# Performance work log

Hardware: AMD Instinct MI355X
Metric: run time of the kernel (lower is better)

The kernel has to match this reference:

```python
import jax, jax.numpy as jnp
import numpy as np

B, S, F_IN, E, H, NIT = 256, 196, 384, 384, 8, 10
FH = E                      # hidden_features defaults to embed_dim
EH = E // H                 # embed dim per head = 48
FHH = FH // H               # hidden features per head = 48
OSEQ = S                    # hidden_seq_len defaults to seq_len
MIN_POS = 1e-6
W_THRESH = 1e-5


def _l1(x, axis=-1, eps=1e-12):
    # F.normalize(p=1): x / max(sum|x|, eps)
    return x / jnp.clip(jnp.sum(jnp.abs(x), axis=axis, keepdims=True), eps, None)


def _norm_weight(w):
    # normalize_weights(): L1-normalize, clamp at threshold, L1-normalize again
    w = _l1(w, axis=-1)
    w = jnp.clip(w, W_THRESH, None)
    return _l1(w, axis=-1)


def setup_inputs() -> dict:
    key = jax.random.key(0)
    ks = jax.random.split(key, 7)
    x = jax.random.normal(ks[0], (B, S, F_IN), dtype=jnp.float32)
    # h init: torch.rand in _reset_h (uniform positive)
    h0 = jax.random.uniform(ks[1], (B, OSEQ, H, FHH), dtype=jnp.float32)
    embed_w = jax.random.normal(ks[2], (E, F_IN), dtype=jnp.float32) * 0.05
    embed_b = jnp.zeros((E,), dtype=jnp.float32)
    local_weight = _norm_weight(jax.random.uniform(ks[3], (FHH, EH), dtype=jnp.float32))
    global_weight = _norm_weight(jax.random.uniform(ks[4], (H, OSEQ, S), dtype=jnp.float32))
    out_w = jax.random.normal(ks[5], (F_IN, E), dtype=jnp.float32) * 0.05
    out_b = jnp.zeros((F_IN,), dtype=jnp.float32)
    return {"x": x, "h0": h0, "embed_w": embed_w, "embed_b": embed_b,
            "local_weight": local_weight, "global_weight": global_weight,
            "out_w": out_w, "out_b": out_b}


def reference(x, h0, embed_w, embed_b, local_weight, global_weight, out_w, out_b):
    # embed + clamp + split heads: [B,S,H,EH]
    xe = jnp.clip(x @ embed_w.T + embed_b, MIN_POS, None)
    xe = xe.reshape(B, S, H, EH)
    # _prepare_input: L1 normalize over last dim (eps=1e-20); nonneg so |x|=x
    inp = xe / jnp.clip(jnp.sum(xe, axis=-1, keepdims=True), 1e-20, None)
    # h init, L1-normalized
    h = _l1(h0, axis=-1)

    def nnmf_forward(t):  # t: [B,S(=i),H,EH]
        t = jnp.einsum('bihe,fe->bihf', t, local_weight)          # F.linear(x, local_weight)
        return jnp.einsum('bihf,hoi->bohf', t, global_weight)     # [B,O,H,FHH]

    def nnmf_reconstruct(hh):  # hh: [B,O,H,FHH]
        t = jnp.einsum('bohf,hoi->bihf', hh, global_weight)
        return jnp.einsum('bihf,fe->bihe', t, local_weight)       # F.linear(., local_weight.t())

    # fixed-point NNMF iterations (h_update_rate=1)
    for _ in range(NIT):
        rec = jnp.clip(nnmf_reconstruct(h), MIN_POS, None)   # secure tensor
        rec = _l1(rec, axis=-1)                              # normalize_reconstruction
        h = h * nnmf_forward(inp / rec)                      # multiplicative update
        h = jnp.clip(h, MIN_POS, None)                       # _secure_tensor
        h = h / jnp.sum(h, axis=-1, keepdims=True)           # PowerSoftmax(power=1)

    # output = 'hidden': flatten heads, project back to features
    out = h.reshape(B, OSEQ, FH)
    return out @ out_w.T + out_b
```

## Files before the change

kernel.cpp:

```cpp
#include <hip/hip_runtime.h>
#include <stdint.h>

#define NB   256
#define NS   196
#define NF   384
#define NH   8
#define NEH  48
#define NIT  10
#define SP   224
#define EP   64
#define NBH  2048
#define NBS  50176
#define NT   13

using f32x4  = __attribute__((ext_vector_type(4))) float;
using u16x8  = __attribute__((ext_vector_type(8))) uint16_t;
using u16x4  = __attribute__((ext_vector_type(4))) uint16_t;
using bf16x8 = __attribute__((ext_vector_type(8))) __bf16;

static __device__ __forceinline__ float bf2f(uint16_t u){
  union { uint32_t u32; float f; } c; c.u32 = (uint32_t)u << 16; return c.f;
}
static __device__ __forceinline__ uint16_t f2bf(float f){
  __bf16 h = (__bf16)f;
  return __builtin_bit_cast(uint16_t, h);
}
static __device__ __forceinline__ float frcp(float f){
  return __builtin_amdgcn_rcpf(f);
}
static __device__ __forceinline__ bf16x8 ld8(const uint16_t* p){
  return __builtin_bit_cast(bf16x8, *(const u16x8*)p);
}
static __device__ __forceinline__ void lds_fence(){
  asm volatile("s_waitcnt lgkmcnt(0)" ::: "memory");
}
static __device__ __forceinline__ float dpp_add16(float x){
  int v = __builtin_bit_cast(int, x);
  x += __builtin_bit_cast(float, __builtin_amdgcn_update_dpp(0, v, 0xB1, 0xF, 0xF, false));
  v = __builtin_bit_cast(int, x);
  x += __builtin_bit_cast(float, __builtin_amdgcn_update_dpp(0, v, 0x4E, 0xF, 0xF, false));
  v = __builtin_bit_cast(int, x);
  x += __builtin_bit_cast(float, __builtin_amdgcn_update_dpp(0, v, 0x141, 0xF, 0xF, false));
  v = __builtin_bit_cast(int, x);
  x += __builtin_bit_cast(float, __builtin_amdgcn_update_dpp(0, v, 0x140, 0xF, 0xF, false));
  return x;
}
#define MFMA16(a,b,c) __builtin_amdgcn_mfma_f32_16x16x32_bf16((a),(b),(c),0,0,0)


__global__ void k_prep_gw(const float* __restrict__ gw, uint16_t* __restrict__ gw_b,
                          uint16_t* __restrict__ gwt_b){
  int idx = blockIdx.x * 256 + threadIdx.x;
  if (idx >= NH*SP*SP) return;
  int h = idx / (SP*SP);
  int r = (idx / SP) % SP;
  int c = idx % SP;
  float v = (r < NS && c < NS) ? gw[((size_t)h*NS + r)*NS + c] : 0.f;
  uint16_t bv = f2bf(v);
  gw_b[idx] = bv;
  gwt_b[((size_t)h*SP + c)*SP + r] = bv;
}

__global__ void k_prep_small(const float* __restrict__ lw, const float* __restrict__ ew,
                             const float* __restrict__ ow,
                             uint16_t* __restrict__ lw_b, uint16_t* __restrict__ lwt_b,
                             uint16_t* __restrict__ ew_b, uint16_t* __restrict__ ow_b){
  int idx = blockIdx.x * 256 + threadIdx.x;
  if (idx < EP*EP){
    int f = idx >> 6, e = idx & 63;
    float v = (f < NEH && e < NEH) ? lw[f*NEH + e] : 0.f;
    uint16_t bv = f2bf(v);
    lw_b[f*EP + e] = bv;
    lwt_b[e*EP + f] = bv;
  }
  if (idx < NF*NF){
    ew_b[idx] = f2bf(ew[idx]);
    ow_b[idx] = f2bf(ow[idx]);
  }
}

__global__ __launch_bounds__(512) void k_embed(const float* __restrict__ x,
    const uint16_t* __restrict__ ew_b, const float* __restrict__ eb,
    uint16_t* __restrict__ inp_fm){
  const int wave = threadIdx.x >> 6, lane = threadIdx.x & 63;
  const int lg = lane >> 4, li = lane & 15;
  const int mt = wave >> 1, nh = wave & 1;
  const int m0 = blockIdx.x * 64 + mt * 16;
  f32x4 acc[12];
  #pragma unroll
  for (int i = 0; i < 12; ++i) acc[i] = (f32x4)0.0f;
  const float* ap = x + (size_t)(m0 + li) * NF + 8*lg;
  for (int kt = 0; kt < 12; ++kt){
    f32x4 a0 = *(const f32x4*)(ap + kt*32);
    f32x4 a1 = *(const f32x4*)(ap + kt*32 + 4);
    u16x8 au;
    #pragma unroll
    for (int j = 0; j < 4; ++j){ au[j] = f2bf(a0[j]); au[j+4] = f2bf(a1[j]); }
    bf16x8 a = __builtin_bit_cast(bf16x8, au);
    #pragma unroll
    for (int nt = 0; nt < 12; ++nt){
      bf16x8 b = ld8(ew_b + (size_t)((nh*12 + nt)*16 + li)*NF + kt*32 + 8*lg);
      acc[nt] = MFMA16(a, b, acc[nt]);
    }
  }
  const int mbase = m0 + 4*lg;
  const int b  = mbase / NS;
  const int si = mbase - b*NS;
  const int t  = si >> 4, wi = si & 15;
  const int lanep = (wi >> 2)*16 + li;
  #pragma unroll
  for (int hl = 0; hl < 4; ++hl){
    int hh = nh*4 + hl;
    float xec[3][4];
    float s[4] = {0.f, 0.f, 0.f, 0.f};
    #pragma unroll
    for (int j = 0; j < 3; ++j){
      int nt = hl*3 + j;
      float bias = eb[(nh*12 + nt)*16 + li];
      #pragma unroll
      for (int r = 0; r < 4; ++r){
        float v = fmaxf(acc[nt][r] + bias, 1e-6f);
        xec[j][r] = v; s[r] += v;
      }
    }
    #pragma unroll
    for (int r = 0; r < 4; ++r) s[r] = frcp(dpp_add16(s[r]));
    uint16_t* dst = inp_fm + ((size_t)((b*NH + hh)*NT + t)*64 + lanep)*12;
    #pragma unroll
    for (int j = 0; j < 3; ++j){
      u16x4 w;
      #pragma unroll
      for (int r = 0; r < 4; ++r) w[r] = f2bf(xec[j][r] * s[r]);
      *(u16x4*)(dst + j*4) = w;
    }
  }
}

__global__ __launch_bounds__(448) void k_main(
    const float*    __restrict__ h0,
    const uint16_t* __restrict__ gw_b,
    const uint16_t* __restrict__ gwt_b,
    const uint16_t* __restrict__ lw_b,
    const uint16_t* __restrict__ lwt_b,
    const uint16_t* __restrict__ inp_fm,
    uint16_t* __restrict__ h_b)
{
  __shared__ __align__(16) uint16_t hlT[48][232];
  __shared__ __align__(16) uint16_t t2T[48][232];
  __shared__ __align__(16) uint16_t Sg[7][2][16][72];

  const int bh = blockIdx.x;
  const int b  = bh >> 3;
  const int hh = bh & 7;
  const int tid = threadIdx.x;
  const int wave = tid >> 6;
  const int lane = tid & 63;
  const int lg = lane >> 4;
  const int li = lane & 15;
  const int tt[2] = {wave, wave + 7};

  {
    u16x4 z = {0,0,0,0};
    *(u16x4*)&Sg[wave][0][li][48 + 4*lg] = z;
    *(u16x4*)&Sg[wave][1][li][48 + 4*lg] = z;
  }

  bf16x8 lwtF[3][2], lwF[3][2];
  #pragma unroll
  for (int nt = 0; nt < 3; ++nt)
    #pragma unroll
    for (int kt = 0; kt < 2; ++kt){
      lwtF[nt][kt] = ld8(lwt_b + (size_t)(nt*16 + li)*EP + kt*32 + 8*lg);
      lwF [nt][kt] = ld8(lw_b  + (size_t)(nt*16 + li)*EP + kt*32 + 8*lg);
    }

  u16x4 ip[2][3];
  #pragma unroll
  for (int tp = 0; tp < 2; ++tp){
    const int t = tt[tp];
    if (t < NT){
      const uint16_t* ipp = inp_fm + ((size_t)(bh*NT + t)*64 + lg*16 + li)*12;
      ip[tp][0] = *(const u16x4*)(ipp);
      ip[tp][1] = *(const u16x4*)(ipp + 4);
      ip[tp][2] = *(const u16x4*)(ipp + 8);
    } else {
      u16x4 z = {0,0,0,0};
      ip[tp][0] = z; ip[tp][1] = z; ip[tp][2] = z;
    }
  }

  float hr[2][3][4];
  #pragma unroll
  for (int tp = 0; tp < 2; ++tp){
    const int t = tt[tp];
    float s[4] = {0.f,0.f,0.f,0.f};
    #pragma unroll
    for (int nt = 0; nt < 3; ++nt)
      #pragma unroll
      for (int r = 0; r < 4; ++r){
        int row = t*16 + 4*lg + r;
        float v = 0.f;
        if (row < NS)
          v = h0[(((size_t)(b*NS + row))*NH + hh)*NEH + nt*16 + li];
        hr[tp][nt][r] = v;
        s[r] += fabsf(v);
      }
    #pragma unroll
    for (int r = 0; r < 4; ++r) s[r] = frcp(fmaxf(dpp_add16(s[r]), 1e-12f));
    #pragma unroll
    for (int nt = 0; nt < 3; ++nt)
      #pragma unroll
      for (int r = 0; r < 4; ++r){
        hr[tp][nt][r] *= s[r];
        Sg[wave][tp][4*lg + r][nt*16 + li] = f2bf(hr[tp][nt][r]);
      }
  }
  lds_fence();
  #pragma unroll
  for (int tp = 0; tp < 2; ++tp){
    const int t = tt[tp];
    f32x4 hl[3];
    #pragma unroll
    for (int i = 0; i < 3; ++i) hl[i] = (f32x4)0.0f;
    #pragma unroll
    for (int kt = 0; kt < 2; ++kt){
      bf16x8 a = ld8(&Sg[wave][tp][li][kt*32 + 8*lg]);
      #pragma unroll
      for (int nt = 0; nt < 3; ++nt) hl[nt] = MFMA16(a, lwtF[nt][kt], hl[nt]);
    }
    #pragma unroll
    for (int nt = 0; nt < 3; ++nt){
      u16x4 w;
      #pragma unroll
      for (int r = 0; r < 4; ++r) w[r] = f2bf(hl[nt][r]);
      *(u16x4*)&hlT[nt*16 + li][t*16 + 4*lg] = w;
    }
  }

  const uint16_t* __restrict__ gwh  = gw_b  + (size_t)hh * SP * SP;
  const uint16_t* __restrict__ gwth = gwt_b + (size_t)hh * SP * SP;
  const uint16_t* gA0t = gwth + (size_t)(tt[0]*16 + li)*SP + 8*lg;
  const uint16_t* gA1t = gwth + (size_t)(tt[1]*16 + li)*SP + 8*lg;
  const uint16_t* gA0  = gwh  + (size_t)(tt[0]*16 + li)*SP + 8*lg;
  const uint16_t* gA1  = gwh  + (size_t)(tt[1]*16 + li)*SP + 8*lg;
  __syncthreads();

  for (int it = 0; it < NIT; ++it){
    f32x4 rec[2][3];
    #pragma unroll
    for (int tp = 0; tp < 2; ++tp)
      #pragma unroll
      for (int i = 0; i < 3; ++i) rec[tp][i] = (f32x4)0.0f;
    #pragma unroll
    for (int kt = 0; kt < 7; ++kt){
      bf16x8 b0 = ld8(&hlT[ 0 + li][kt*32 + 8*lg]);
      bf16x8 b1 = ld8(&hlT[16 + li][kt*32 + 8*lg]);
      bf16x8 b2 = ld8(&hlT[32 + li][kt*32 + 8*lg]);
      bf16x8 a0 = ld8(gA0t + kt*32);
      bf16x8 a1 = ld8(gA1t + kt*32);
      rec[0][0] = MFMA16(a0, b0, rec[0][0]);
      rec[0][1] = MFMA16(a0, b1, rec[0][1]);
      rec[0][2] = MFMA16(a0, b2, rec[0][2]);
      rec[1][0] = MFMA16(a1, b0, rec[1][0]);
      rec[1][1] = MFMA16(a1, b1, rec[1][1]);
      rec[1][2] = MFMA16(a1, b2, rec[1][2]);
    }
    #pragma unroll
    for (int tp = 0; tp < 2; ++tp){
      float s[4] = {0.f,0.f,0.f,0.f};
      float rv[3][4];
      #pragma unroll
      for (int nt = 0; nt < 3; ++nt)
        #pragma unroll
        for (int r = 0; r < 4; ++r){
          float v = fmaxf(rec[tp][nt][r], 1e-6f);
          rv[nt][r] = v; s[r] += v;
        }
      #pragma unroll
      for (int r = 0; r < 4; ++r) s[r] = dpp_add16(s[r]);
      #pragma unroll
      for (int r = 0; r < 4; ++r){
        Sg[wave][tp][4*lg + r][ 0 + li] = f2bf(bf2f(ip[tp][0][r]) * s[r] * frcp(rv[0][r]));
        Sg[wave][tp][4*lg + r][16 + li] = f2bf(bf2f(ip[tp][1][r]) * s[r] * frcp(rv[1][r]));
        Sg[wave][tp][4*lg + r][32 + li] = f2bf(bf2f(ip[tp][2][r]) * s[r] * frcp(rv[2][r]));
      }
    }
    lds_fence();
    #pragma unroll
    for (int tp = 0; tp < 2; ++tp){
      const int t = tt[tp];
      f32x4 t2[3];
      #pragma unroll
      for (int i = 0; i < 3; ++i) t2[i] = (f32x4)0.0f;
      #pragma unroll
      for (int kt = 0; kt < 2; ++kt){
        bf16x8 a = ld8(&Sg[wave][tp][li][kt*32 + 8*lg]);
        #pragma unroll
        for (int nt = 0; nt < 3; ++nt) t2[nt] = MFMA16(a, lwF[nt][kt], t2[nt]);
      }
      #pragma unroll
      for (int nt = 0; nt < 3; ++nt){
        u16x4 w;
        #pragma unroll
        for (int r = 0; r < 4; ++r) w[r] = f2bf(t2[nt][r]);
        *(u16x4*)&t2T[nt*16 + li][t*16 + 4*lg] = w;
      }
    }
    __syncthreads();

    f32x4 hu[2][3];
    #pragma unroll
    for (int tp = 0; tp < 2; ++tp)
      #pragma unroll
      for (int i = 0; i < 3; ++i) hu[tp][i] = (f32x4)0.0f;
    #pragma unroll
    for (int kt = 0; kt < 7; ++kt){
      bf16x8 b0 = ld8(&t2T[ 0 + li][kt*32 + 8*lg]);
      bf16x8 b1 = ld8(&t2T[16 + li][kt*32 + 8*lg]);
      bf16x8 b2 = ld8(&t2T[32 + li][kt*32 + 8*lg]);
      bf16x8 a0 = ld8(gA0 + kt*32);
      bf16x8 a1 = ld8(gA1 + kt*32);
      hu[0][0] = MFMA16(a0, b0, hu[0][0]);
      hu[0][1] = MFMA16(a0, b1, hu[0][1]);
      hu[0][2] = MFMA16(a0, b2, hu[0][2]);
      hu[1][0] = MFMA16(a1, b0, hu[1][0]);
      hu[1][1] = MFMA16(a1, b1, hu[1][1]);
      hu[1][2] = MFMA16(a1, b2, hu[1][2]);
    }
    #pragma unroll
    for (int tp = 0; tp < 2; ++tp){
      float s[4] = {0.f,0.f,0.f,0.f};
      #pragma unroll
      for (int nt = 0; nt < 3; ++nt)
        #pragma unroll
        for (int r = 0; r < 4; ++r){
          float v = fmaxf(hr[tp][nt][r] * hu[tp][nt][r], 1e-6f);
          hr[tp][nt][r] = v; s[r] += v;
        }
      #pragma unroll
      for (int r = 0; r < 4; ++r) s[r] = frcp(dpp_add16(s[r]));
      #pragma unroll
      for (int nt = 0; nt < 3; ++nt)
        #pragma unroll
        for (int r = 0; r < 4; ++r){
          hr[tp][nt][r] *= s[r];
          Sg[wave][tp][4*lg + r][nt*16 + li] = f2bf(hr[tp][nt][r]);
        }
    }
    lds_fence();
    #pragma unroll
    for (int tp = 0; tp < 2; ++tp){
      const int t = tt[tp];
      f32x4 hl[3];
      #pragma unroll
      for (int i = 0; i < 3; ++i) hl[i] = (f32x4)0.0f;
      #pragma unroll
      for (int kt = 0; kt < 2; ++kt){
        bf16x8 a = ld8(&Sg[wave][tp][li][kt*32 + 8*lg]);
        #pragma unroll
        for (int nt = 0; nt < 3; ++nt) hl[nt] = MFMA16(a, lwtF[nt][kt], hl[nt]);
      }
      #pragma unroll
      for (int nt = 0; nt < 3; ++nt){
        u16x4 w;
        #pragma unroll
        for (int r = 0; r < 4; ++r) w[r] = f2bf(hl[nt][r]);
        *(u16x4*)&hlT[nt*16 + li][t*16 + 4*lg] = w;
      }
    }
    __syncthreads();
  }

  uint16_t* __restrict__ hrow = h_b + (size_t)bh * SP * EP;
  #pragma unroll
  for (int tp = 0; tp < 2; ++tp){
    const int t = tt[tp];
    #pragma unroll
    for (int nt = 0; nt < 3; ++nt)
      #pragma unroll
      for (int r = 0; r < 4; ++r){
        int row = t*16 + 4*lg + r;
        if (row < NS)
          hrow[(size_t)row*EP + nt*16 + li] = f2bf(hr[tp][nt][r]);
      }
  }
}

__global__ __launch_bounds__(512) void k_out(const uint16_t* __restrict__ h_b,
    const uint16_t* __restrict__ ow_b, const float* __restrict__ obv,
    float* __restrict__ out){
  const int wave = threadIdx.x >> 6, lane = threadIdx.x & 63;
  const int lg = lane >> 4, li = lane & 15;
  const int p = wave >> 2, q = wave & 3;
  const int m0 = blockIdx.x * 64;
  f32x4 acc[2][6];
  #pragma unroll
  for (int mtl = 0; mtl < 2; ++mtl)
    #pragma unroll
    for (int i = 0; i < 6; ++i) acc[mtl][i] = (f32x4)0.0f;
  size_t rowbase[2];
  #pragma unroll
  for (int mtl = 0; mtl < 2; ++mtl){
    int m = m0 + (2*p + mtl)*16 + li;
    int b = m / NS, si = m - b*NS;
    rowbase[mtl] = ((size_t)b*NH*SP + si)*EP;
  }
  for (int kt = 0; kt < 12; ++kt){
    int ks = kt*32 + 8*lg;
    int hh = ks / NEH, f = ks - hh*NEH;
    size_t koff = (size_t)hh*SP*EP + f;
    bf16x8 a0 = ld8(h_b + rowbase[0] + koff);
    bf16x8 a1 = ld8(h_b + rowbase[1] + koff);
    #pragma unroll
    for (int n = 0; n < 6; ++n){
      bf16x8 bb = ld8(ow_b + (size_t)((6*q + n)*16 + li)*NF + kt*32 + 8*lg);
      acc[0][n] = MFMA16(a0, bb, acc[0][n]);
      acc[1][n] = MFMA16(a1, bb, acc[1][n]);
    }
  }
  #pragma unroll
  for (int mtl = 0; mtl < 2; ++mtl){
    #pragma unroll
    for (int n = 0; n < 6; ++n){
      int col = (6*q + n)*16 + li;
      float bias = obv[col];
      #pragma unroll
      for (int r = 0; r < 4; ++r)
        out[(size_t)(m0 + (2*p + mtl)*16 + 4*lg + r)*NF + col] = acc[mtl][n][r] + bias;
    }
  }
}

extern "C" void kernel_launch(void* const* d_in, const int* in_sizes, int n_in,
                              void* d_out, int out_size, void* d_ws, size_t ws_size,
                              hipStream_t stream){
  const float* x   = (const float*)d_in[0];
  const float* h0  = (const float*)d_in[1];
  const float* ew  = (const float*)d_in[2];
  const float* eb  = (const float*)d_in[3];
  const float* lw  = (const float*)d_in[4];
  const float* gw  = (const float*)d_in[5];
  const float* ow  = (const float*)d_in[6];
  const float* obv = (const float*)d_in[7];
  float* out = (float*)d_out;

  char* w = (char*)d_ws;
  size_t o_inp = 0;
  size_t o_hb  = o_inp + (size_t)NBH*NT*64*12*2;
  size_t o_gw  = o_hb  + (size_t)NBH*SP*EP*2;
  size_t o_gwt = o_gw  + (size_t)NH*SP*SP*2;
  size_t o_lw  = o_gwt + (size_t)NH*SP*SP*2;
  size_t o_lwt = o_lw  + (size_t)EP*EP*2;
  size_t o_ew  = o_lwt + (size_t)EP*EP*2;
  size_t o_ow  = o_ew  + (size_t)NF*NF*2;
  size_t total = o_ow  + (size_t)NF*NF*2;
  if (ws_size < total) return;

  uint16_t* inp_fm = (uint16_t*)(w + o_inp);
  uint16_t* h_b    = (uint16_t*)(w + o_hb);
  uint16_t* gw_b   = (uint16_t*)(w + o_gw);
  uint16_t* gwt_b  = (uint16_t*)(w + o_gwt);
  uint16_t* lw_b   = (uint16_t*)(w + o_lw);
  uint16_t* lwt_b  = (uint16_t*)(w + o_lwt);
  uint16_t* ew_b   = (uint16_t*)(w + o_ew);
  uint16_t* ow_b   = (uint16_t*)(w + o_ow);

  k_prep_gw<<<(NH*SP*SP + 255)/256, 256, 0, stream>>>(gw, gw_b, gwt_b);
  k_prep_small<<<(NF*NF + 255)/256, 256, 0, stream>>>(lw, ew, ow, lw_b, lwt_b, ew_b, ow_b);
  k_embed<<<NBS/64, 512, 0, stream>>>(x, ew_b, eb, inp_fm);
  k_main<<<NBH, 448, 0, stream>>>(h0, gw_b, gwt_b, lw_b, lwt_b, inp_fm, h_b);
  k_out<<<NBS/64, 512, 0, stream>>>(h_b, ow_b, obv, out);
}
```

Before: 658.8 us.

## Pack two batch items per workgroup in NNMF main kernel

The main iteration kernel now runs two (batch, head) pairs per workgroup with 896 threads, doubling the shared buffers and indexing them by half. Both halves share the same head, so their global_weight reads may hit cache together, and the launch count is halved. In exchange, barriers now synchronise 14 waves instead of 7, LDS per block doubles, and the 896-thread launch bound may raise register pressure. Waves past index 7 in Sg are addressed by the full wave index, so that indexing appears consistent.

```diff
diff --git a/kernel.cpp b/kernel.cpp
--- a/kernel.cpp
+++ b/kernel.cpp
@@ -136,7 +136,7 @@
   }
 }
 
-__global__ __launch_bounds__(448) void k_main(
+__global__ __launch_bounds__(896) void k_main(
     const float*    __restrict__ h0,
     const uint16_t* __restrict__ gw_b,
     const uint16_t* __restrict__ gwt_b,
@@ -145,19 +145,22 @@
     const uint16_t* __restrict__ inp_fm,
     uint16_t* __restrict__ h_b)
 {
-  __shared__ __align__(16) uint16_t hlT[48][232];
-  __shared__ __align__(16) uint16_t t2T[48][232];
-  __shared__ __align__(16) uint16_t Sg[7][2][16][72];
-
-  const int bh = blockIdx.x;
-  const int b  = bh >> 3;
-  const int hh = bh & 7;
+  __shared__ __align__(16) uint16_t hlT[2][48][232];
+  __shared__ __align__(16) uint16_t t2T[2][48][232];
+  __shared__ __align__(16) uint16_t Sg[14][2][16][72];
+
+  const int hh = blockIdx.x & 7;
+  const int bp = blockIdx.x >> 3;
   const int tid = threadIdx.x;
   const int wave = tid >> 6;
+  const int half = (wave >= 7) ? 1 : 0;
+  const int wl   = wave - half*7;
+  const int b    = bp*2 + half;
+  const int bh   = b*NH + hh;
   const int lane = tid & 63;
   const int lg = lane >> 4;
   const int li = lane & 15;
-  const int tt[2] = {wave, wave + 7};
+  const int tt[2] = {wl, wl + 7};
 
   {
     u16x4 z = {0,0,0,0};
@@ -233,7 +236,7 @@
       u16x4 w;
       #pragma unroll
       for (int r = 0; r < 4; ++r) w[r] = f2bf(hl[nt][r]);
-      *(u16x4*)&hlT[nt*16 + li][t*16 + 4*lg] = w;
+      *(u16x4*)&hlT[half][nt*16 + li][t*16 + 4*lg] = w;
     }
   }
 
@@ -253,9 +256,9 @@
       for (int i = 0; i < 3; ++i) rec[tp][i] = (f32x4)0.0f;
     #pragma unroll
     for (int kt = 0; kt < 7; ++kt){
-      bf16x8 b0 = ld8(&hlT[ 0 + li][kt*32 + 8*lg]);
-      bf16x8 b1 = ld8(&hlT[16 + li][kt*32 + 8*lg]);
-      bf16x8 b2 = ld8(&hlT[32 + li][kt*32 + 8*lg]);
+      bf16x8 b0 = ld8(&hlT[half][ 0 + li][kt*32 + 8*lg]);
+      bf16x8 b1 = ld8(&hlT[half][16 + li][kt*32 + 8*lg]);
+      bf16x8 b2 = ld8(&hlT[half][32 + li][kt*32 + 8*lg]);
       bf16x8 a0 = ld8(gA0t + kt*32);
       bf16x8 a1 = ld8(gA1t + kt*32);
       rec[0][0] = MFMA16(a0, b0, rec[0][0]);
@@ -303,7 +306,7 @@
         u16x4 w;
         #pragma unroll
         for (int r = 0; r < 4; ++r) w[r] = f2bf(t2[nt][r]);
-        *(u16x4*)&t2T[nt*16 + li][t*16 + 4*lg] = w;
+        *(u16x4*)&t2T[half][nt*16 + li][t*16 + 4*lg] = w;
       }
     }
     __syncthreads();
@@ -315,9 +318,9 @@
       for (int i = 0; i < 3; ++i) hu[tp][i] = (f32x4)0.0f;
     #pragma unroll
     for (int kt = 0; kt < 7; ++kt){
-      bf16x8 b0 = ld8(&t2T[ 0 + li][kt*32 + 8*lg]);
-      bf16x8 b1 = ld8(&t2T[16 + li][kt*32 + 8*lg]);
-      bf16x8 b2 = ld8(&t2T[32 + li][kt*32 + 8*lg]);
+      bf16x8 b0 = ld8(&t2T[half][ 0 + li][kt*32 + 8*lg]);
+      bf16x8 b1 = ld8(&t2T[half][16 + li][kt*32 + 8*lg]);
+      bf16x8 b2 = ld8(&t2T[half][32 + li][kt*32 + 8*lg]);
       bf16x8 a0 = ld8(gA0 + kt*32);
       bf16x8 a1 = ld8(gA1 + kt*32);
       hu[0][0] = MFMA16(a0, b0, hu[0][0]);
@@ -365,7 +368,7 @@
         u16x4 w;
         #pragma unroll
         for (int r = 0; r < 4; ++r) w[r] = f2bf(hl[nt][r]);
-        *(u16x4*)&hlT[nt*16 + li][t*16 + 4*lg] = w;
+        *(u16x4*)&hlT[half][nt*16 + li][t*16 + 4*lg] = w;
       }
     }
     __syncthreads();
@@ -468,6 +471,6 @@
   k_prep_gw<<<(NH*SP*SP + 255)/256, 256, 0, stream>>>(gw, gw_b, gwt_b);
   k_prep_small<<<(NF*NF + 255)/256, 256, 0, stream>>>(lw, ew, ow, lw_b, lwt_b, ew_b, ow_b);
   k_embed<<<NBS/64, 512, 0, stream>>>(x, ew_b, eb, inp_fm);
-  k_main<<<NBH, 448, 0, stream>>>(h0, gw_b, gwt_b, lw_b, lwt_b, inp_fm, h_b);
+  k_main<<<NBH/2, 896, 0, stream>>>(h0, gw_b, gwt_b, lw_b, lwt_b, inp_fm, h_b);
   k_out<<<NBS/64, 512, 0, stream>>>(h_b, ow_b, obv, out);
 }
```

Measured after the change: 1.196 ms. +81.5%, slower.
